# Kernel optimization log

Measured on AMD Instinct MI355X. Metric: run time of the kernel, lower is better.

## Reference

```python
import jax, jax.numpy as jnp
import numpy as np

B, C, H, W = 16, 192, 56, 56   # feature map from visual encoder
K = 9                          # kNN neighbors (knn_graph k)
NUM_CLASSES = 100
PRED_DIM = 1024                # pred_emb_dim
EPS = 1e-5                     # BatchNorm eps


def setup_inputs() -> dict:
    key = jax.random.key(0)
    ks = jax.random.split(key, 6)
    def kaiming(k, shape, fan_in):
        return jax.random.normal(k, shape, jnp.float32) * np.float32(np.sqrt(2.0 / fan_in))
    return {
        "image_feature_map": jax.random.normal(ks[0], (B, C, H, W), jnp.float32),
        # 1x1 conv patch-prediction head: Conv2d(C, NUM_CLASSES, 1)
        "conv_w": kaiming(ks[1], (NUM_CLASSES, C), C),
        "conv_b": jnp.zeros((NUM_CLASSES,), jnp.float32),
        # stand-in for opaque GSAT GNN: one linear + mean neighbor aggregation
        "gnn_w": kaiming(ks[2], (C, C), C),
        "gnn_b": jnp.zeros((C,), jnp.float32),
        # prediction head: Linear(C, PRED_DIM) -> BN -> GELU -> Linear(PRED_DIM, NUM_CLASSES)
        "w1": kaiming(ks[3], (C, PRED_DIM), C),
        "b1": jnp.zeros((PRED_DIM,), jnp.float32),
        "bn_gamma": jnp.ones((PRED_DIM,), jnp.float32),
        "bn_beta": jnp.zeros((PRED_DIM,), jnp.float32),
        "w2": kaiming(ks[4], (PRED_DIM, NUM_CLASSES), PRED_DIM),
        "b2": jnp.zeros((NUM_CLASSES,), jnp.float32),
    }


def _knn_edges(x_norm):
    """x_norm: [B, N, C] L2-normalized. Per-image kNN (no cross-batch edges,
    no self loops). Returns global (src, dst) of shape [B*N*K] each,
    src = neighbor, dst = center node (PyG source_to_target flow)."""
    N = x_norm.shape[1]
    # normalized vectors: argmin Euclidean dist == argmax cosine sim
    sim = jnp.einsum('bnc,bmc->bnm', x_norm, x_norm)          # [B,N,N]
    sim = sim - 4.0 * jnp.eye(N, dtype=sim.dtype)             # exclude self
    _, nbr = jax.lax.top_k(sim, K)                            # [B,N,K]
    offs = (jnp.arange(B) * N)[:, None, None]
    src = (nbr + offs).reshape(-1)
    dst = (jnp.broadcast_to(jnp.arange(N)[None, :, None], (B, N, K)) + offs).reshape(-1)
    return src, dst


def reference(image_feature_map, conv_w, conv_b, gnn_w, gnn_b,
              w1, b1, bn_gamma, bn_beta, w2, b2):
    N = H * W
    # patch predictions: 1x1 conv over feature map
    patch_pred = jnp.einsum('bchw,kc->bkhw', image_feature_map, conv_w) + conv_b[None, :, None, None]
    # reshape_into_graph_input: [B,C,H,W] -> [B*N, C] nodes, then L2 normalize
    x = image_feature_map.reshape(B, C, N).transpose(0, 2, 1)  # [B,N,C]
    x = x / jnp.maximum(jnp.linalg.norm(x, axis=-1, keepdims=True), 1e-12)
    # knn_graph under no_grad
    src, dst = _knn_edges(jax.lax.stop_gradient(x))
    nodes = x.reshape(B * N, C)
    # GNN stand-in: linear + relu, edge attention, mean neighbor aggregation
    h = jax.nn.relu(nodes @ gnn_w + gnn_b)                     # [B*N, C]
    raw_edge_att = jnp.sum(h[src] * h[dst], axis=-1)           # [B*N*K]
    edge_att = jax.nn.sigmoid(raw_edge_att)
    msg = jax.ops.segment_sum(h[src], dst, num_segments=B * N)
    h = h + msg / np.float32(K)
    # global_add_pool over batch assignment
    batch = jnp.repeat(jnp.arange(B), N)
    g = jax.ops.segment_sum(h, batch, num_segments=B)          # [B, C]
    # prediction MLP: Linear -> BatchNorm1d (train-mode batch stats) -> GELU -> Linear
    z = g @ w1 + b1
    mu = jnp.mean(z, axis=0)
    var = jnp.var(z, axis=0)
    z = (z - mu) * jax.lax.rsqrt(var + EPS) * bn_gamma + bn_beta
    z = jax.nn.gelu(z, approximate=False)
    pred = z @ w2 + b2                                         # [B, NUM_CLASSES]
    return (pred, edge_att, patch_pred)
```

## Files before the change

### kernel.cpp

```cpp
#include <hip/hip_runtime.h>
#include <math.h>

#define B_  16
#define C_  192
#define N_  3136
#define BN_ 50176
#define K_  9
#define NC_ 100
#define PD_ 1024
#define NSEV 7
#define SEVCOLS 448

#define OUT_EATT 1600
#define OUT_PP   453184

typedef short bf16x8 __attribute__((ext_vector_type(8)));
typedef float f32x16 __attribute__((ext_vector_type(16)));

__device__ __forceinline__ unsigned int umaxu(unsigned int a, unsigned int b) { return a > b ? a : b; }
__device__ __forceinline__ unsigned int med3u(unsigned int a, unsigned int b, unsigned int c) {
    unsigned int d;
    asm("v_med3_u32 %0, %1, %2, %3" : "=v"(d) : "v"(a), "v"(b), "v"(c));
    return d;
}
__device__ __forceinline__ void ins12m(unsigned int (&lk)[12], unsigned int key) {
    unsigned int nk[12];
    nk[0] = umaxu(lk[0], key);
    #pragma unroll
    for (int k = 1; k < 12; ++k) nk[k] = med3u(lk[k - 1], lk[k], key);
    #pragma unroll
    for (int k = 0; k < 12; ++k) lk[k] = nk[k];
}

template<int NL>
__device__ inline void ins_lex(float (&lv)[NL], int (&li)[NL], float v, int vi) {
    if (v > lv[NL-1] || (v == lv[NL-1] && vi < li[NL-1])) {
        #pragma unroll
        for (int k = 0; k < NL; ++k) {
            bool p = (v > lv[k]) || (v == lv[k] && vi < li[k]);
            float fv = p ? lv[k] : v; int fi = p ? li[k] : vi;
            lv[k] = p ? v : lv[k];    li[k] = p ? vi : li[k];
            v = fv; vi = fi;
        }
    }
}

__device__ inline unsigned int bf16_rne(unsigned int u) {
    return (u + 0x7fffu + ((u >> 16) & 1u)) & 0xffff0000u;
}

__global__ __launch_bounds__(256) void k_normalize(const float* __restrict__ in,
        float* __restrict__ xn, unsigned short* __restrict__ xsn,
        float* __restrict__ norms) {
    __shared__ float tile[C_][65];
    __shared__ float part[4][64];
    __shared__ float rnorm_s[64];
    int b = blockIdx.x & 15;
    int n0 = (blockIdx.x >> 4) * 64;
    int t = threadIdx.x;
    for (int f = t; f < C_ * 64; f += 256) {
        int c = f >> 6, n = f & 63;
        tile[c][n] = in[((size_t)b * C_ + c) * N_ + n0 + n];
    }
    __syncthreads();
    {
        int n = t & 63, qq = t >> 6;
        float s = 0.f;
        #pragma unroll
        for (int i = 0; i < 48; ++i) { float v = tile[qq * 48 + i][n]; s += v * v; }
        part[qq][n] = s;
    }
    __syncthreads();
    if (t < 64) {
        float tot = part[0][t] + part[1][t] + part[2][t] + part[3][t];
        float nrm = fmaxf(sqrtf(tot), 1e-12f);
        norms[(size_t)b * N_ + n0 + t] = nrm;
        rnorm_s[t] = 1.0f / nrm;
    }
    __syncthreads();
    for (int f = t; f < 64 * 96; f += 256) {
        int n = f / 96, cp = f - n * 96;
        int c = cp * 2;
        float r = rnorm_s[n];
        float v0 = tile[c][n] * r;
        float v1 = tile[c + 1][n] * r;
        size_t row = (size_t)b * N_ + n0 + n;
        *(float2*)(xn + row * C_ + c) = make_float2(v0, v1);
        unsigned int h0 = bf16_rne(__float_as_uint(v0));
        unsigned int h1 = bf16_rne(__float_as_uint(v1));
        unsigned int l0 = bf16_rne(__float_as_uint(v0 - __uint_as_float(h0)));
        unsigned int l1 = bf16_rne(__float_as_uint(v1 - __uint_as_float(h1)));
        unsigned int* xr = (unsigned int*)(xsn + row * 384);
        xr[cp]      = (h0 >> 16) | (h1 & 0xffff0000u);
        xr[96 + cp] = (l0 >> 16) | (l1 & 0xffff0000u);
    }
}

__global__ __launch_bounds__(256) void k_wsplit(const float* __restrict__ cw,
        const float* __restrict__ gw, const float* __restrict__ w2,
        unsigned short* __restrict__ wsc, unsigned short* __restrict__ wsg,
        float* __restrict__ w2t) {
    int id = blockIdx.x * 256 + threadIdx.x;
    if (id < 128 * 192) {
        int k = id / 192, c = id - k * 192;
        float v = (k < 100) ? cw[k * 192 + c] : 0.f;
        unsigned int h = bf16_rne(__float_as_uint(v));
        wsc[(size_t)k * 384 + c] = (unsigned short)(h >> 16);
        wsc[(size_t)k * 384 + 192 + c] =
            (unsigned short)(bf16_rne(__float_as_uint(v - __uint_as_float(h))) >> 16);
    } else if (id < 61440) {
        int e = id - 128 * 192;
        int cc = e / 192, j = e - cc * 192;
        float v = gw[cc * 192 + j];
        unsigned int h = bf16_rne(__float_as_uint(v));
        wsg[(size_t)j * 384 + cc] = (unsigned short)(h >> 16);
        wsg[(size_t)j * 384 + 192 + cc] =
            (unsigned short)(bf16_rne(__float_as_uint(v - __uint_as_float(h))) >> 16);
    } else {
        int e2 = id - 61440;
        int jj = e2 >> 10, k = e2 & 1023;
        w2t[(size_t)jj * PD_ + k] = w2[(size_t)k * NC_ + jj];
    }
}

#define STAGE32(DST, SRCBASE, NLW) { \
    const char* s_ = (SRCBASE); \
    _Pragma("unroll") \
    for (int q_ = 0; q_ < NLW; ++q_) \
        __builtin_amdgcn_global_load_lds( \
            (const __attribute__((address_space(1))) unsigned int*)(s_ + q_ * 32), \
            (__attribute__((address_space(3))) unsigned int*)((DST) + (w * NLW + q_) * 1024), 16, 0, 0); }

#define STAGEHALF(DST, BASE, COLB, KH, NLW) { \
    _Pragma("unroll") \
    for (int q_ = 0; q_ < NLW; ++q_) { \
        const char* s_ = (BASE) + (size_t)((COLB) + l31) * 768 + (KH) * 384 + (w * (NLW) + q_) * 32 + lh * 16; \
        __builtin_amdgcn_global_load_lds( \
            (const __attribute__((address_space(1))) unsigned int*)s_, \
            (__attribute__((address_space(3))) unsigned int*)((DST) + (w * (NLW) + q_) * 1024), 16, 0, 0); } }

#define SCAN16 { \
    int c0 = cbase + c * 32 + 4 * lh; \
    int kc = 4095 - c0; \
    _Pragma("unroll") \
    for (int g = 0; g < 4; ++g) { \
        _Pragma("unroll") \
        for (int q = 0; q < 4; ++q) { \
            unsigned int u = __float_as_uint(fmaf(acc[4 * g + q], 0.125f, 0.75f)); \
            unsigned int key = ((u >> 3) << 12) | (unsigned int)(kc - (8 * g + q)); \
            ins12m(lk, key); \
        } \
    } }
#define SCAN16D { \
    int c0 = cbase + c * 32 + 4 * lh; \
    int selfslot = r - c0; \
    int kc = 4095 - c0; \
    _Pragma("unroll") \
    for (int g = 0; g < 4; ++g) { \
        _Pragma("unroll") \
        for (int q = 0; q < 4; ++q) { \
            unsigned int u = __float_as_uint(fmaf(acc[4 * g + q], 0.125f, 0.75f)); \
            unsigned int key = ((u >> 3) << 12) | (unsigned int)(kc - (8 * g + q)); \
            key = (8 * g + q == selfslot) ? 0u : key; \
            ins12m(lk, key); \
        } \
    } }

__global__ __launch_bounds__(256, 3) void k_simmfma(const unsigned short* __restrict__ xs,
        unsigned int* __restrict__ topk) {
    __shared__ __align__(1024) char SMEM[24576];
    int bid = blockIdx.x;
    int img = bid & 15;
    int rest = bid >> 4;
    int rb = rest / NSEV;
    int sv = rest - rb * NSEV;
    int t = threadIdx.x;
    int w = t >> 6, lane = t & 63;
    int l31 = lane & 31, lh = lane >> 5;
    const char* xsi = (const char*)(xs + (size_t)img * N_ * 384);

    int r = rb * 128 + w * 32 + l31;
    bool valid = r < N_;
    int rl = valid ? r : (N_ - 1);
    bf16x8 bfrag[24];
    {
        const char* rp = xsi + (size_t)rl * 768 + lh * 16;
        #pragma unroll
        for (int ks = 0; ks < 24; ++ks)
            bfrag[ks] = *(const bf16x8*)(rp + ks * 32);
    }
    unsigned int lk[12];
    #pragma unroll
    for (int k = 0; k < 12; ++k) lk[k] = 0u;

    int cbase = sv * SEVCOLS;
    int c_self = rb * 4 + w - sv * 14;

    STAGEHALF(SMEM, xsi, cbase, 0, 3)
    __syncthreads();

    for (int c = 0; c < 14; ++c) {
        STAGEHALF(SMEM + 12288, xsi, cbase + c * 32, 1, 3)
        f32x16 acc;
        #pragma unroll
        for (int i = 0; i < 16; ++i) acc[i] = 0.f;
        {
            const char* rp = SMEM + lh * 512 + l31 * 16;
            __builtin_amdgcn_s_setprio(1);
            #pragma unroll
            for (int ks = 0; ks < 12; ++ks) {
                bf16x8 af = *(const bf16x8*)(rp + ks * 1024);
                acc = __builtin_amdgcn_mfma_f32_32x32x16_bf16(af, bfrag[ks], acc, 0, 0, 0);
            }
            __builtin_amdgcn_s_setprio(0);
        }
        __syncthreads();
        if (c < 13) { STAGEHALF(SMEM, xsi, cbase + (c + 1) * 32, 0, 3) }
        {
            const char* rp = SMEM + 12288 + lh * 512 + l31 * 16;
            __builtin_amdgcn_s_setprio(1);
            #pragma unroll
            for (int ks = 0; ks < 12; ++ks) {
                bf16x8 af = *(const bf16x8*)(rp + ks * 1024);
                acc = __builtin_amdgcn_mfma_f32_32x32x16_bf16(af, bfrag[12 + ks], acc, 0, 0, 0);
            }
            __builtin_amdgcn_s_setprio(0);
        }
        if (valid) {
            if (c == c_self) SCAN16D
            else             SCAN16
        }
        __syncthreads();
    }
    unsigned int pk[12];
    #pragma unroll
    for (int j = 0; j < 12; ++j)
        pk[j] = (unsigned int)__shfl_xor((int)lk[j], 32, 64);
    #pragma unroll
    for (int j = 0; j < 12; ++j) ins12m(lk, pk[j]);
    if (valid && lh == 0) {
        unsigned int* op = topk + ((size_t)sv * BN_ + (size_t)img * N_ + r) * 12;
        #pragma unroll
        for (int k = 0; k < 12; ++k) op[k] = lk[k];
    }
}

__global__ __launch_bounds__(256, 3) void k_patchmfma(const unsigned short* __restrict__ xs,
        const unsigned short* __restrict__ wsc, const float* __restrict__ norms,
        const float* __restrict__ cb, float* __restrict__ outp) {
    __shared__ __align__(1024) char SMEM[24576];
    int bid = blockIdx.x;
    int img = bid & 15;
    int n0 = (bid >> 4) * 64;
    int t = threadIdx.x;
    int w = t >> 6, lane = t & 63;
    int l31 = lane & 31, lh = lane >> 5;
    const char* xsi = (const char*)(xs + (size_t)img * N_ * 384);
    int ch = w * 32 + l31;
    bf16x8 bfrag[24];
    {
        const char* wp = (const char*)wsc + (size_t)ch * 768 + lh * 16;
        #pragma unroll
        for (int ks = 0; ks < 24; ++ks)
            bfrag[ks] = *(const bf16x8*)(wp + ks * 32);
    }
    float bias = (ch < NC_) ? cb[ch] : 0.f;
    STAGEHALF(SMEM, xsi, n0, 0, 3)
    __syncthreads();
    for (int c = 0; c < 2; ++c) {
        STAGEHALF(SMEM + 12288, xsi, n0 + c * 32, 1, 3)
        f32x16 acc;
        #pragma unroll
        for (int i = 0; i < 16; ++i) acc[i] = 0.f;
        {
            const char* rp = SMEM + lh * 512 + l31 * 16;
            #pragma unroll
            for (int ks = 0; ks < 12; ++ks) {
                bf16x8 af = *(const bf16x8*)(rp + ks * 1024);
                acc = __builtin_amdgcn_mfma_f32_32x32x16_bf16(af, bfrag[ks], acc, 0, 0, 0);
            }
        }
        __syncthreads();
        if (c == 0) { STAGEHALF(SMEM, xsi, n0 + 32, 0, 3) }
        {
            const char* rp = SMEM + 12288 + lh * 512 + l31 * 16;
            #pragma unroll
            for (int ks = 0; ks < 12; ++ks) {
                bf16x8 af = *(const bf16x8*)(rp + ks * 1024);
                acc = __builtin_amdgcn_mfma_f32_32x32x16_bf16(af, bfrag[12 + ks], acc, 0, 0, 0);
            }
        }
        if (ch < NC_) {
            int nb = n0 + c * 32 + 4 * lh;
            float* op = outp + ((size_t)(img * NC_ + ch)) * N_ + nb;
            const float* npv = norms + (size_t)img * N_ + nb;
            #pragma unroll
            for (int g = 0; g < 4; ++g) {
                float4 nv = *(const float4*)(npv + 8 * g);
                float4 o;
                o.x = acc[4 * g + 0] * nv.x + bias;
                o.y = acc[4 * g + 1] * nv.y + bias;
                o.z = acc[4 * g + 2] * nv.z + bias;
                o.w = acc[4 * g + 3] * nv.w + bias;
                *(float4*)(op + 8 * g) = o;
            }
        }
        __syncthreads();
    }
}

__global__ __launch_bounds__(384, 3) void k_gnnmfma(const unsigned short* __restrict__ xs,
        const unsigned short* __restrict__ wsg, const float* __restrict__ gbias,
        float* __restrict__ h) {
    __shared__ __align__(1024) char SMEM[49152];
    int n0 = blockIdx.x * 128;
    int t = threadIdx.x;
    int w = t / 64, lane = t & 63;
    int l31 = lane & 31, lh = lane >> 5;
    int j = w * 32 + l31;
    bf16x8 bfrag[24];
    {
        const char* wp = (const char*)wsg + (size_t)j * 768 + lh * 16;
        #pragma unroll
        for (int ks = 0; ks < 24; ++ks)
            bfrag[ks] = *(const bf16x8*)(wp + ks * 32);
    }
    float bj = gbias[j];
    STAGE32(SMEM, (const char*)xs + (size_t)(n0 + l31) * 768 + w * 128 + lh * 16, 4);
    __syncthreads();
    for (int c = 0; c < 4; ++c) {
        char* cur = SMEM + (c & 1) * 24576;
        if (c < 3) {
            char* dst = SMEM + ((c & 1) ^ 1) * 24576;
            STAGE32(dst, (const char*)xs + (size_t)(n0 + (c + 1) * 32 + l31) * 768 + w * 128 + lh * 16, 4);
        }
        f32x16 acc;
        #pragma unroll
        for (int i = 0; i < 16; ++i) acc[i] = 0.f;
        const char* rp = cur + lh * 512 + l31 * 16;
        #pragma unroll
        for (int ks = 0; ks < 24; ++ks) {
            bf16x8 af = *(const bf16x8*)(rp + ks * 1024);
            acc = __builtin_amdgcn_mfma_f32_32x32x16_bf16(af, bfrag[ks], acc, 0, 0, 0);
        }
        int nb = n0 + c * 32 + 4 * lh;
        #pragma unroll
        for (int g = 0; g < 4; ++g)
            #pragma unroll
            for (int q = 0; q < 4; ++q)
                h[(size_t)(nb + 8 * g + q) * C_ + j] = fmaxf(acc[4 * g + q] + bj, 0.f);
        __syncthreads();
    }
}

__global__ __launch_bounds__(256) void k_merge2(const unsigned int* __restrict__ topk,
        int* __restrict__ nbr12) {
    int row = blockIdx.x * 256 + threadIdx.x;
    unsigned int lk[12];
    const unsigned int* p0 = topk + (size_t)row * 12;
    #pragma unroll
    for (int k = 0; k < 12; ++k) lk[k] = p0[k];
    #pragma unroll
    for (int h = 1; h < NSEV; ++h) {
        const unsigned int* p1 = topk + ((size_t)h * BN_ + row) * 12;
        #pragma unroll
        for (int j = 0; j < 12; ++j) ins12m(lk, p1[j]);
    }
    int gb = (row / N_) * N_;
    int* np = nbr12 + (size_t)row * 12;
    #pragma unroll
    for (int k = 0; k < 12; ++k) np[k] = gb + (4095 - (int)(lk[k] & 0xFFFu));
}

__global__ __launch_bounds__(256) void k_rescore(const float* __restrict__ xn,
        const int* __restrict__ nbr12, int* __restrict__ nbr9) {
    int img = blockIdx.x & 15;
    int sub = blockIdx.x >> 4;
    int t = threadIdx.x;
    int nl = t >> 4, l16 = t & 15;
    int row = img * N_ + sub * 16 + nl;
    const float4* xa = (const float4*)(xn + (size_t)row * C_) + l16;
    float4 a0 = xa[0], a1 = xa[16], a2 = xa[32];
    const int* np12 = nbr12 + (size_t)row * 12;
    float d[12]; int ci[12];
    #pragma unroll
    for (int j = 0; j < 12; ++j) {
        int cand = np12[j];
        ci[j] = cand;
        const float4* xb = (const float4*)(xn + (size_t)cand * C_) + l16;
        float4 b0 = xb[0], b1 = xb[16], b2 = xb[32];
        float s = a0.x*b0.x + a0.y*b0.y + a0.z*b0.z + a0.w*b0.w
                + a1.x*b1.x + a1.y*b1.y + a1.z*b1.z + a1.w*b1.w
                + a2.x*b2.x + a2.y*b2.y + a2.z*b2.z + a2.w*b2.w;
        s += __shfl_xor(s, 1, 64);
        s += __shfl_xor(s, 2, 64);
        s += __shfl_xor(s, 4, 64);
        s += __shfl_xor(s, 8, 64);
        d[j] = (cand != row) ? s : -1e30f;
    }
    float lv[9]; int li[9];
    #pragma unroll
    for (int k = 0; k < 9; ++k) { lv[k] = -1e30f; li[k] = 0x7fffffff; }
    #pragma unroll
    for (int j = 0; j < 12; ++j) ins_lex<9>(lv, li, d[j], ci[j]);
    if (l16 == 0) {
        int* np = nbr9 + (size_t)row * 9;
        #pragma unroll
        for (int k = 0; k < 9; ++k) np[k] = li[k];
    }
}

__global__ __launch_bounds__(256) void k_edge(const float* __restrict__ h,
        const int* __restrict__ nbr, float* __restrict__ eatt,
        float* __restrict__ gparte) {
    __shared__ float ps[4][C_];
    int img = blockIdx.x & 15;
    int sub = blockIdx.x >> 4;
    int t = threadIdx.x;
    int wv = t >> 6;
    int nl = t >> 4;
    int l16 = t & 15;
    int node = img * N_ + sub * 16 + nl;
    const float4* hc = (const float4*)(h + (size_t)node * C_) + l16;
    float4 c0 = hc[0], c1 = hc[16], c2 = hc[32];
    float4 m0 = make_float4(0,0,0,0), m1 = make_float4(0,0,0,0), m2 = make_float4(0,0,0,0);
    const int* np_ = nbr + (size_t)node * K_;
    float* ep = eatt + (size_t)node * K_;
    #pragma unroll
    for (int k = 0; k < K_; ++k) {
        int src = np_[k];
        const float4* hs = (const float4*)(h + (size_t)src * C_) + l16;
        float4 s0 = hs[0], s1 = hs[16], s2 = hs[32];
        float d = s0.x*c0.x + s0.y*c0.y + s0.z*c0.z + s0.w*c0.w
                + s1.x*c1.x + s1.y*c1.y + s1.z*c1.z + s1.w*c1.w
                + s2.x*c2.x + s2.y*c2.y + s2.z*c2.z + s2.w*c2.w;
        d += __shfl_xor(d, 1, 64);
        d += __shfl_xor(d, 2, 64);
        d += __shfl_xor(d, 4, 64);
        d += __shfl_xor(d, 8, 64);
        if (l16 == 0) ep[k] = 1.0f / (1.0f + expf(-d));
        m0.x += s0.x; m0.y += s0.y; m0.z += s0.z; m0.w += s0.w;
        m1.x += s1.x; m1.y += s1.y; m1.z += s1.z; m1.w += s1.w;
        m2.x += s2.x; m2.y += s2.y; m2.z += s2.z; m2.w += s2.w;
    }
    const float r9 = 1.0f / 9.0f;
    float v[12];
    v[0] = c0.x + m0.x * r9; v[1]  = c0.y + m0.y * r9;
    v[2] = c0.z + m0.z * r9; v[3]  = c0.w + m0.w * r9;
    v[4] = c1.x + m1.x * r9; v[5]  = c1.y + m1.y * r9;
    v[6] = c1.z + m1.z * r9; v[7]  = c1.w + m1.w * r9;
    v[8] = c2.x + m2.x * r9; v[9]  = c2.y + m2.y * r9;
    v[10] = c2.z + m2.z * r9; v[11] = c2.w + m2.w * r9;
    #pragma unroll
    for (int e = 0; e < 12; ++e) {
        v[e] += __shfl_xor(v[e], 16, 64);
        v[e] += __shfl_xor(v[e], 32, 64);
    }
    if ((t & 63) < 16) {
        #pragma unroll
        for (int j = 0; j < 3; ++j)
            #pragma unroll
            for (int e = 0; e < 4; ++e)
                ps[wv][j * 64 + l16 * 4 + e] = v[j * 4 + e];
    }
    __syncthreads();
    if (t < C_)
        gparte[(size_t)blockIdx.x * C_ + t] =
            (ps[0][t] + ps[1][t]) + (ps[2][t] + ps[3][t]);
}

__global__ __launch_bounds__(192) void k_gred(const float* __restrict__ gparte,
        float* __restrict__ gpart) {
    int b = blockIdx.x >> 2, s = blockIdx.x & 3;
    int oc = threadIdx.x;
    float acc = 0.f;
    for (int sub = s * 49; sub < (s + 1) * 49; ++sub)
        acc += gparte[((size_t)(sub * 16 + b)) * C_ + oc];
    gpart[(size_t)(b * 4 + s) * C_ + oc] = acc;
}

__global__ __launch_bounds__(256) void k_mlp1(const float* __restrict__ gpart,
        const float* __restrict__ w1, const float* __restrict__ b1,
        const float* __restrict__ gam, const float* __restrict__ bet,
        float* __restrict__ zs) {
    __shared__ float gs[B_ * C_];
    int t = threadIdx.x;
    int j = blockIdx.x * 256 + t;
    for (int f = t; f < B_ * C_; f += 256) {
        int b = f / C_, oc = f - b * C_;
        float a = 0.f;
        #pragma unroll
        for (int s = 0; s < 4; ++s) a += gpart[((size_t)(b * 4 + s)) * C_ + oc];
        gs[f] = a;
    }
    __syncthreads();
    float z[16];
    #pragma unroll
    for (int i = 0; i < 16; ++i) z[i] = b1[j];
    for (int c = 0; c < C_; ++c) {
        float w = w1[(size_t)c * PD_ + j];
        #pragma unroll
        for (int i = 0; i < 16; ++i) z[i] += gs[i * C_ + c] * w;
    }
    float mu = 0.f;
    #pragma unroll
    for (int i = 0; i < 16; ++i) mu += z[i];
    mu *= (1.0f / 16.0f);
    float var = 0.f;
    #pragma unroll
    for (int i = 0; i < 16; ++i) { float d = z[i] - mu; var += d * d; }
    var *= (1.0f / 16.0f);
    float sc = (1.0f / sqrtf(var + 1e-5f)) * gam[j];
    float bt = bet[j];
    #pragma unroll
    for (int i = 0; i < 16; ++i) {
        float zh = (z[i] - mu) * sc + bt;
        zs[(size_t)i * PD_ + j] = 0.5f * zh * (1.0f + erff(zh * 0.70710678118654752f));
    }
}

__global__ __launch_bounds__(64) void k_mlp2(const float* __restrict__ zs,
        const float* __restrict__ w2t, const float* __restrict__ b2,
        float* __restrict__ pred) {
    int i = blockIdx.x / NC_, jj = blockIdx.x - i * NC_;
    int lane = threadIdx.x;
    const float* zr = zs + (size_t)i * PD_;
    const float* wr = w2t + (size_t)jj * PD_;
    float a = 0.f;
    #pragma unroll
    for (int k = 0; k < 16; ++k) a += zr[lane + 64 * k] * wr[lane + 64 * k];
    a += __shfl_xor(a, 1, 64);  a += __shfl_xor(a, 2, 64);
    a += __shfl_xor(a, 4, 64);  a += __shfl_xor(a, 8, 64);
    a += __shfl_xor(a, 16, 64); a += __shfl_xor(a, 32, 64);
    if (lane == 0) pred[i * NC_ + jj] = a + b2[jj];
}

extern "C" void kernel_launch(void* const* d_in, const int* in_sizes, int n_in,
                              void* d_out, int out_size, void* d_ws, size_t ws_size,
                              hipStream_t stream) {
    const float* img    = (const float*)d_in[0];
    const float* conv_w = (const float*)d_in[1];
    const float* conv_b = (const float*)d_in[2];
    const float* gnn_w  = (const float*)d_in[3];
    const float* gnn_b  = (const float*)d_in[4];
    const float* w1     = (const float*)d_in[5];
    const float* b1     = (const float*)d_in[6];
    const float* bng    = (const float*)d_in[7];
    const float* bnb    = (const float*)d_in[8];
    const float* w2     = (const float*)d_in[9];
    const float* b2     = (const float*)d_in[10];
    float* out = (float*)d_out;

    float* XN            = (float*)d_ws;
    unsigned short* XS   = (unsigned short*)(XN + (size_t)BN_ * C_);
    unsigned int* TOPK   = (unsigned int*)(XS + (size_t)BN_ * 384);
    int*   NBR12         = (int*)(TOPK + (size_t)NSEV * BN_ * 12);
    int*   NBR9          = NBR12 + (size_t)BN_ * 12;
    float* NORMS         = (float*)(NBR9 + (size_t)BN_ * K_);
    unsigned short* WSC  = (unsigned short*)(NORMS + BN_);
    unsigned short* WSG  = WSC + (size_t)128 * 384;
    float* GPART         = (float*)(WSG + (size_t)192 * 384);
    float* W2T           = GPART + (size_t)128 * C_;
    float* Hh            = XN;
    float* GPARTE        = (float*)TOPK;
    float* ZS            = (float*)NBR12;

    k_normalize<<<784, 256, 0, stream>>>(img, XN, XS, NORMS);
    k_wsplit   <<<640, 256, 0, stream>>>(conv_w, gnn_w, w2, WSC, WSG, W2T);
    k_patchmfma<<<784, 256, 0, stream>>>(XS, WSC, NORMS, conv_b, out + OUT_PP);
    k_simmfma  <<<2800, 256, 0, stream>>>(XS, TOPK);
    k_merge2   <<<196, 256, 0, stream>>>(TOPK, NBR12);
    k_rescore  <<<3136, 256, 0, stream>>>(XN, NBR12, NBR9);
    k_gnnmfma  <<<392, 384, 0, stream>>>(XS, WSG, gnn_b, Hh);
    k_edge     <<<3136, 256, 0, stream>>>(Hh, NBR9, out + OUT_EATT, GPARTE);
    k_gred     <<<64, 192, 0, stream>>>(GPARTE, GPART);
    k_mlp1     <<<4, 256, 0, stream>>>(GPART, w1, b1, bng, bnb, ZS);
    k_mlp2     <<<1600, 64, 0, stream>>>(ZS, W2T, b2, out);
}
```

Before: 361.7 us.

## Store split-bf16 features in MFMA-tile-swizzled layout for contiguous LDS staging

The normalize kernel now writes the hi/lo bf16 feature copies in a pre-tiled layout: 32-row tiles, each holding a 12 KB hi half and a 12 KB lo half arranged exactly as the MFMA LDS fragments expect. The similarity, patch and GNN kernels then stage tiles with fully contiguous 16-byte-per-lane global-to-LDS loads instead of row-strided gathers, and the similarity kernel reads its register fragments from the same layout. This aims to cut scattered global accesses in the dominant kNN similarity kernel. In exchange, the normalize kernel's stores become more scattered, and every consumer depends on the new indexing being correct.

```diff
diff --git a/kernel.cpp b/kernel.cpp
--- a/kernel.cpp
+++ b/kernel.cpp
@@ -10,6 +10,8 @@
 #define PD_ 1024
 #define NSEV 7
 #define SEVCOLS 448
+#define TILEB 24576
+#define HALFB 12288
 
 #define OUT_EATT 1600
 #define OUT_PP   453184
@@ -49,8 +51,9 @@
     return (u + 0x7fffu + ((u >> 16) & 1u)) & 0xffff0000u;
 }
 
+
 __global__ __launch_bounds__(256) void k_normalize(const float* __restrict__ in,
-        float* __restrict__ xn, unsigned short* __restrict__ xsn,
+        float* __restrict__ xn, char* __restrict__ xs2,
         float* __restrict__ norms) {
     __shared__ float tile[C_][65];
     __shared__ float part[4][64];
@@ -84,15 +87,17 @@
         float r = rnorm_s[n];
         float v0 = tile[c][n] * r;
         float v1 = tile[c + 1][n] * r;
-        size_t row = (size_t)b * N_ + n0 + n;
-        *(float2*)(xn + row * C_ + c) = make_float2(v0, v1);
+        int row = b * N_ + n0 + n;
+        *(float2*)(xn + (size_t)row * C_ + c) = make_float2(v0, v1);
         unsigned int h0 = bf16_rne(__float_as_uint(v0));
         unsigned int h1 = bf16_rne(__float_as_uint(v1));
         unsigned int l0 = bf16_rne(__float_as_uint(v0 - __uint_as_float(h0)));
         unsigned int l1 = bf16_rne(__float_as_uint(v1 - __uint_as_float(h1)));
-        unsigned int* xr = (unsigned int*)(xsn + row * 384);
-        xr[cp]      = (h0 >> 16) | (h1 & 0xffff0000u);
-        xr[96 + cp] = (l0 >> 16) | (l1 & 0xffff0000u);
+        int cb = row >> 5, l31 = row & 31;
+        int ks = cp >> 3, lh = (cp >> 2) & 1, off = 4 * (cp & 3);
+        char* base = xs2 + (size_t)cb * TILEB + ks * 1024 + lh * 512 + l31 * 16 + off;
+        *(unsigned int*)base           = (h0 >> 16) | (h1 & 0xffff0000u);
+        *(unsigned int*)(base + HALFB) = (l0 >> 16) | (l1 & 0xffff0000u);
     }
 }
 
@@ -123,18 +128,17 @@
     }
 }
 
-#define STAGE32(DST, SRCBASE, NLW) { \
-    const char* s_ = (SRCBASE); \
-    _Pragma("unroll") \
-    for (int q_ = 0; q_ < NLW; ++q_) \
-        __builtin_amdgcn_global_load_lds( \
-            (const __attribute__((address_space(1))) unsigned int*)(s_ + q_ * 32), \
-            (__attribute__((address_space(3))) unsigned int*)((DST) + (w * NLW + q_) * 1024), 16, 0, 0); }
-
-#define STAGEHALF(DST, BASE, COLB, KH, NLW) { \
+#define STAGETILE(DST, BASE, CB, KH, NLW) { \
     _Pragma("unroll") \
     for (int q_ = 0; q_ < NLW; ++q_) { \
-        const char* s_ = (BASE) + (size_t)((COLB) + l31) * 768 + (KH) * 384 + (w * (NLW) + q_) * 32 + lh * 16; \
+        const char* s_ = (BASE) + (size_t)(CB) * TILEB + (KH) * HALFB + (w * (NLW) + q_) * 1024 + lane * 16; \
+        __builtin_amdgcn_global_load_lds( \
+            (const __attribute__((address_space(1))) unsigned int*)s_, \
+            (__attribute__((address_space(3))) unsigned int*)((DST) + (w * (NLW) + q_) * 1024), 16, 0, 0); } }
+#define STAGEPAIR(DST, BASE, CB, NLW) { \
+    _Pragma("unroll") \
+    for (int q_ = 0; q_ < NLW; ++q_) { \
+        const char* s_ = (BASE) + (size_t)(CB) * TILEB + (w * (NLW) + q_) * 1024 + lane * 16; \
         __builtin_amdgcn_global_load_lds( \
             (const __attribute__((address_space(1))) unsigned int*)s_, \
             (__attribute__((address_space(3))) unsigned int*)((DST) + (w * (NLW) + q_) * 1024), 16, 0, 0); } }
@@ -166,7 +170,7 @@
         } \
     } }
 
-__global__ __launch_bounds__(256, 3) void k_simmfma(const unsigned short* __restrict__ xs,
+__global__ __launch_bounds__(256, 3) void k_simmfma(const char* __restrict__ xs2,
         unsigned int* __restrict__ topk) {
     __shared__ __align__(1024) char SMEM[24576];
     int bid = blockIdx.x;
@@ -177,17 +181,20 @@
     int t = threadIdx.x;
     int w = t >> 6, lane = t & 63;
     int l31 = lane & 31, lh = lane >> 5;
-    const char* xsi = (const char*)(xs + (size_t)img * N_ * 384);
+    const char* xsi = xs2 + (size_t)img * 98 * TILEB;
 
     int r = rb * 128 + w * 32 + l31;
     bool valid = r < N_;
-    int rl = valid ? r : (N_ - 1);
+    int cbr = rb * 4 + w;
+    if (cbr > 97) cbr = 97;
     bf16x8 bfrag[24];
     {
-        const char* rp = xsi + (size_t)rl * 768 + lh * 16;
-        #pragma unroll
-        for (int ks = 0; ks < 24; ++ks)
-            bfrag[ks] = *(const bf16x8*)(rp + ks * 32);
+        const char* rp = xsi + (size_t)cbr * TILEB + lh * 512 + l31 * 16;
+        #pragma unroll
+        for (int kh = 0; kh < 2; ++kh)
+            #pragma unroll
+            for (int ks = 0; ks < 12; ++ks)
+                bfrag[kh * 12 + ks] = *(const bf16x8*)(rp + kh * HALFB + ks * 1024);
     }
     unsigned int lk[12];
     #pragma unroll
@@ -196,11 +203,11 @@
     int cbase = sv * SEVCOLS;
     int c_self = rb * 4 + w - sv * 14;
 
-    STAGEHALF(SMEM, xsi, cbase, 0, 3)
+    STAGETILE(SMEM, xsi, sv * 14, 0, 3)
     __syncthreads();
 
     for (int c = 0; c < 14; ++c) {
-        STAGEHALF(SMEM + 12288, xsi, cbase + c * 32, 1, 3)
+        STAGETILE(SMEM + HALFB, xsi, sv * 14 + c, 1, 3)
         f32x16 acc;
         #pragma unroll
         for (int i = 0; i < 16; ++i) acc[i] = 0.f;
@@ -215,9 +222,9 @@
             __builtin_amdgcn_s_setprio(0);
         }
         __syncthreads();
-        if (c < 13) { STAGEHALF(SMEM, xsi, cbase + (c + 1) * 32, 0, 3) }
+        if (c < 13) { STAGETILE(SMEM, xsi, sv * 14 + c + 1, 0, 3) }
         {
-            const char* rp = SMEM + 12288 + lh * 512 + l31 * 16;
+            const char* rp = SMEM + HALFB + lh * 512 + l31 * 16;
             __builtin_amdgcn_s_setprio(1);
             #pragma unroll
             for (int ks = 0; ks < 12; ++ks) {
@@ -245,9 +252,9 @@
     }
 }
 
-__global__ __launch_bounds__(256, 3) void k_patchmfma(const unsigned short* __restrict__ xs,
+__global__ __launch_bounds__(256, 3) void k_patchmfma(const char* __restrict__ xs2,
         const unsigned short* __restrict__ wsc, const float* __restrict__ norms,
-        const float* __restrict__ cb, float* __restrict__ outp) {
+        const float* __restrict__ cb_, float* __restrict__ outp) {
     __shared__ __align__(1024) char SMEM[24576];
     int bid = blockIdx.x;
     int img = bid & 15;
@@ -255,7 +262,7 @@
     int t = threadIdx.x;
     int w = t >> 6, lane = t & 63;
     int l31 = lane & 31, lh = lane >> 5;
-    const char* xsi = (const char*)(xs + (size_t)img * N_ * 384);
+    const char* xsi = xs2 + (size_t)img * 98 * TILEB;
     int ch = w * 32 + l31;
     bf16x8 bfrag[24];
     {
@@ -264,11 +271,11 @@
         for (int ks = 0; ks < 24; ++ks)
             bfrag[ks] = *(const bf16x8*)(wp + ks * 32);
     }
-    float bias = (ch < NC_) ? cb[ch] : 0.f;
-    STAGEHALF(SMEM, xsi, n0, 0, 3)
+    float bias = (ch < NC_) ? cb_[ch] : 0.f;
+    STAGETILE(SMEM, xsi, n0 >> 5, 0, 3)
     __syncthreads();
     for (int c = 0; c < 2; ++c) {
-        STAGEHALF(SMEM + 12288, xsi, n0 + c * 32, 1, 3)
+        STAGETILE(SMEM + HALFB, xsi, (n0 >> 5) + c, 1, 3)
         f32x16 acc;
         #pragma unroll
         for (int i = 0; i < 16; ++i) acc[i] = 0.f;
@@ -281,9 +288,9 @@
             }
         }
         __syncthreads();
-        if (c == 0) { STAGEHALF(SMEM, xsi, n0 + 32, 0, 3) }
+        if (c == 0) { STAGETILE(SMEM, xsi, (n0 >> 5) + 1, 0, 3) }
         {
-            const char* rp = SMEM + 12288 + lh * 512 + l31 * 16;
+            const char* rp = SMEM + HALFB + lh * 512 + l31 * 16;
             #pragma unroll
             for (int ks = 0; ks < 12; ++ks) {
                 bf16x8 af = *(const bf16x8*)(rp + ks * 1024);
@@ -309,7 +316,7 @@
     }
 }
 
-__global__ __launch_bounds__(384, 3) void k_gnnmfma(const unsigned short* __restrict__ xs,
+__global__ __launch_bounds__(384, 3) void k_gnnmfma(const char* __restrict__ xs2,
         const unsigned short* __restrict__ wsg, const float* __restrict__ gbias,
         float* __restrict__ h) {
     __shared__ __align__(1024) char SMEM[49152];
@@ -326,22 +333,27 @@
             bfrag[ks] = *(const bf16x8*)(wp + ks * 32);
     }
     float bj = gbias[j];
-    STAGE32(SMEM, (const char*)xs + (size_t)(n0 + l31) * 768 + w * 128 + lh * 16, 4);
+    STAGEPAIR(SMEM, xs2, n0 >> 5, 4)
     __syncthreads();
     for (int c = 0; c < 4; ++c) {
         char* cur = SMEM + (c & 1) * 24576;
         if (c < 3) {
             char* dst = SMEM + ((c & 1) ^ 1) * 24576;
-            STAGE32(dst, (const char*)xs + (size_t)(n0 + (c + 1) * 32 + l31) * 768 + w * 128 + lh * 16, 4);
+            STAGEPAIR(dst, xs2, (n0 >> 5) + c + 1, 4)
         }
         f32x16 acc;
         #pragma unroll
         for (int i = 0; i < 16; ++i) acc[i] = 0.f;
         const char* rp = cur + lh * 512 + l31 * 16;
         #pragma unroll
-        for (int ks = 0; ks < 24; ++ks) {
+        for (int ks = 0; ks < 12; ++ks) {
             bf16x8 af = *(const bf16x8*)(rp + ks * 1024);
             acc = __builtin_amdgcn_mfma_f32_32x32x16_bf16(af, bfrag[ks], acc, 0, 0, 0);
+        }
+        #pragma unroll
+        for (int ks = 0; ks < 12; ++ks) {
+            bf16x8 af = *(const bf16x8*)(rp + HALFB + ks * 1024);
+            acc = __builtin_amdgcn_mfma_f32_32x32x16_bf16(af, bfrag[12 + ks], acc, 0, 0, 0);
         }
         int nb = n0 + c * 32 + 4 * lh;
         #pragma unroll
@@ -552,8 +564,8 @@
     float* out = (float*)d_out;
 
     float* XN            = (float*)d_ws;
-    unsigned short* XS   = (unsigned short*)(XN + (size_t)BN_ * C_);
-    unsigned int* TOPK   = (unsigned int*)(XS + (size_t)BN_ * 384);
+    char*  XS2           = (char*)(XN + (size_t)BN_ * C_);
+    unsigned int* TOPK   = (unsigned int*)(XS2 + (size_t)BN_ * 768);
     int*   NBR12         = (int*)(TOPK + (size_t)NSEV * BN_ * 12);
     int*   NBR9          = NBR12 + (size_t)BN_ * 12;
     float* NORMS         = (float*)(NBR9 + (size_t)BN_ * K_);
@@ -565,13 +577,13 @@
     float* GPARTE        = (float*)TOPK;
     float* ZS            = (float*)NBR12;
 
-    k_normalize<<<784, 256, 0, stream>>>(img, XN, XS, NORMS);
+    k_normalize<<<784, 256, 0, stream>>>(img, XN, XS2, NORMS);
     k_wsplit   <<<640, 256, 0, stream>>>(conv_w, gnn_w, w2, WSC, WSG, W2T);
-    k_patchmfma<<<784, 256, 0, stream>>>(XS, WSC, NORMS, conv_b, out + OUT_PP);
-    k_simmfma  <<<2800, 256, 0, stream>>>(XS, TOPK);
+    k_patchmfma<<<784, 256, 0, stream>>>(XS2, WSC, NORMS, conv_b, out + OUT_PP);
+    k_simmfma  <<<2800, 256, 0, stream>>>(XS2, TOPK);
     k_merge2   <<<196, 256, 0, stream>>>(TOPK, NBR12);
     k_rescore  <<<3136, 256, 0, stream>>>(XN, NBR12, NBR9);
-    k_gnnmfma  <<<392, 384, 0, stream>>>(XS, WSG, gnn_b, Hh);
+    k_gnnmfma  <<<392, 384, 0, stream>>>(XS2, WSG, gnn_b, Hh);
     k_edge     <<<3136, 256, 0, stream>>>(Hh, NBR9, out + OUT_EATT, GPARTE);
     k_gred     <<<64, 192, 0, stream>>>(GPARTE, GPART);
     k_mlp1     <<<4, 256, 0, stream>>>(GPART, w1, b1, bng, bnb, ZS);
```

New measurement: 347.5 us. 3.9% less time.
